# Kernel tuning notes

Hardware: AMD Instinct MI355X
Metric: run time of the kernel (lower is better)

The kernel has to match this reference:

```python
import jax, jax.numpy as jnp
import numpy as np
import math

EPS = 0.0001

def _filterbank(delta, center, image_size, glimpse_size):
    # delta, center: (B,) in [-1,1]. Returns (B, glimpse_size, image_size),
    # matching torch _get_filterbanks output fx.transpose(1,2).
    centers = (image_size - 1.0) * (center + 1.0) / 2.0            # (B,)
    deltas = (float(image_size) / glimpse_size) * (1.0 - jnp.abs(delta))
    gammas = jnp.exp(1.0 - 2.0 * jnp.abs(delta))                   # (B,)
    gp = jnp.arange(glimpse_size, dtype=jnp.float32) - (glimpse_size - 1.0) / 2.0
    mu = centers[:, None] + deltas[:, None] * gp[None, :]          # (B, g)
    ip = jnp.arange(image_size, dtype=jnp.float32)                 # (I,)
    fx = (ip[None, None, :] - mu[:, :, None]) / gammas[:, None, None]  # (B, g, I)
    fx = 1.0 / (math.pi * gammas[:, None, None] * (1.0 + fx * fx))
    fx = fx / (jnp.sum(fx, axis=2, keepdims=True) + EPS)
    return fx


def setup_inputs() -> dict:
    key = jax.random.key(0)
    ks = jax.random.split(key, 7)
    B, C, H, W = 64, 3, 256, 256
    gh, gw, co = 16, 16, 512
    in_dim = gh * gw * C
    s_ih = 1.0 / np.sqrt(co)
    return {
        "image_pairs": jax.random.normal(ks[0], (B, 2, C, H, W), dtype=jnp.float32),
        "W_ih": jax.random.normal(ks[1], (4 * co, in_dim), dtype=jnp.float32) * s_ih,
        "W_hh": jax.random.normal(ks[2], (4 * co, co), dtype=jnp.float32) * s_ih,
        "b_ih": jax.random.normal(ks[3], (4 * co,), dtype=jnp.float32) * s_ih,
        "b_hh": jax.random.normal(ks[4], (4 * co,), dtype=jnp.float32) * s_ih,
        "Wg": jax.random.normal(ks[5], (3, co), dtype=jnp.float32) * 0.05,
        "bg": jax.random.normal(ks[6], (3,), dtype=jnp.float32) * 0.05,
        "num_glimpses": 8,
    }


def reference(image_pairs, W_ih, W_hh, b_ih, b_hh, Wg, bg, num_glimpses):
    B, _, C, H, W = image_pairs.shape
    co = W_hh.shape[1]
    gh = gw = 16

    def step(carry, turn):
        h, c = carry
        img = image_pairs[:, turn % 2]                 # (B, C, H, W)
        gp = jnp.tanh(h @ Wg.T + bg)                   # (B, 3)
        Fh = _filterbank(gp[:, 2], gp[:, 0], H, gh)    # (B, gh, H)
        Fw = _filterbank(gp[:, 2], gp[:, 1], W, gw)    # (B, gw, W)
        # glimpse = Fh @ img @ Fw^T per channel -> (B, C, gh, gw)
        g = jnp.einsum('bgh,bchw->bcgw', Fh, img)
        g = jnp.einsum('bcgw,bkw->bcgk', g, Fw)
        x = g.reshape(B, -1)                           # (B, C*gh*gw)
        gates = x @ W_ih.T + b_ih + h @ W_hh.T + b_hh  # (B, 4*co)
        i, f, gg, o = jnp.split(gates, 4, axis=1)
        c_new = jax.nn.sigmoid(f) * c + jax.nn.sigmoid(i) * jnp.tanh(gg)
        h_new = jax.nn.sigmoid(o) * jnp.tanh(c_new)
        return (h_new, c_new), h_new

    h0 = jnp.zeros((B, co), dtype=jnp.float32)
    c0 = jnp.zeros((B, co), dtype=jnp.float32)
    (hT, _), _ = jax.lax.scan(step, (h0, c0), jnp.arange(2 * num_glimpses))
    return hT
```

## Files before the change

kernel.cpp:

```cpp
#include <hip/hip_runtime.h>
#include <math.h>

#define NB 64
#define CO 512
#define NGATES 2048
#define INDIM 768
#define KTOT 1280
#define IMG 256
#define GS 16
#define EPSF 1e-4f
#define NCHUNK 8
#define CHUNK 160

#define FMA4(A,S,V) {(A).x+=(S)*(V).x;(A).y+=(S)*(V).y;(A).z+=(S)*(V).z;(A).w+=(S)*(V).w;}

__device__ __forceinline__ float sigmoidf_(float x){ return 1.0f/(1.0f+expf(-x)); }

__device__ __forceinline__ float waveReduceSum(float v){
  #pragma unroll
  for (int off=32; off>0; off>>=1) v += __shfl_down(v, off, 64);
  return v;
}

__global__ __launch_bounds__(256) void transpose_k(const float* __restrict__ in,
                                                   float* __restrict__ out,
                                                   int rows, int cols){
  __shared__ float tile[32][33];
  int bx = blockIdx.x*32, by = blockIdx.y*32;
  int tx = threadIdx.x, ty = threadIdx.y;
  #pragma unroll
  for (int i=ty;i<32;i+=8)
    tile[i][tx] = in[(size_t)(by+i)*cols + bx+tx];
  __syncthreads();
  #pragma unroll
  for (int i=ty;i<32;i+=8)
    out[(size_t)(bx+i)*rows + by+tx] = tile[tx][i];
}

__global__ __launch_bounds__(512) void extlstm4_k(
    const float* __restrict__ imgs, int t,
    const float* __restrict__ partT,
    const float* __restrict__ b_ih, const float* __restrict__ b_hh,
    const float* __restrict__ Wg,   const float* __restrict__ bg,
    float* __restrict__ cbuf, float* __restrict__ xhT)
{
  __shared__ float hs[CO];
  __shared__ float gp[3];
  __shared__ float wred[8][4];
  __shared__ float prt[2][GS][4];
  __shared__ float rowinv[2][GS];
  __shared__ float fhT[256][20];
  __shared__ float fws[GS][260];
  __shared__ float g1[4][GS][260];
  __shared__ float g2[256][2];

  const int bc = blockIdx.x;
  const int b = bc/3, c = bc%3;
  const int t0 = threadIdx.x;
  const int q = t0>>6, lane = t0&63;

  if (t == 0){
    if (t0 < 256){ hs[t0]=0.f; hs[t0+256]=0.f; }
    if (c == 0) xhT[(size_t)(INDIM+t0)*NB + b] = 0.f;
  } else {
    const int u = t0;
    float gi=0.f,gf=0.f,gc=0.f,go=0.f;
    #pragma unroll
    for (int s2=0;s2<NCHUNK;s2++){
      const float* p = partT + ((size_t)s2*NB + b)*NGATES;
      gi += p[u]; gf += p[512+u]; gc += p[1024+u]; go += p[1536+u];
    }
    gi += b_ih[u]      + b_hh[u];
    gf += b_ih[512+u]  + b_hh[512+u];
    gc += b_ih[1024+u] + b_hh[1024+u];
    go += b_ih[1536+u] + b_hh[1536+u];
    float cold = (t==1) ? 0.f : cbuf[(size_t)((t-1)&1)*NB*CO + (size_t)b*CO + u];
    float cnew = sigmoidf_(gf)*cold + sigmoidf_(gi)*tanhf(gc);
    float hnew = sigmoidf_(go)*tanhf(cnew);
    hs[u] = hnew;
    if (c == 0){
      cbuf[(size_t)(t&1)*NB*CO + (size_t)b*CO + u] = cnew;
      xhT[(size_t)(INDIM+u)*NB + b] = hnew;
    }
  }
  __syncthreads();

  {
    float hval = hs[t0];
    float p0 = Wg[0*CO+t0]*hval;
    float p1 = Wg[1*CO+t0]*hval;
    float p2 = Wg[2*CO+t0]*hval;
    p0 = waveReduceSum(p0); p1 = waveReduceSum(p1); p2 = waveReduceSum(p2);
    if (lane==0){ wred[q][0]=p0; wred[q][1]=p1; wred[q][2]=p2; }
    __syncthreads();
    if (t0 < 3){
      float s = 0.f;
      #pragma unroll
      for (int w8=0; w8<8; w8++) s += wred[w8][t0];
      gp[t0] = tanhf(s + bg[t0]);
    }
    __syncthreads();
  }

  {
    float delta = gp[2];
    float dabs  = fabsf(delta);
    float deltas = ((float)IMG/(float)GS) * (1.0f - dabs);
    float gamma  = expf(1.0f - 2.0f*dabs);
    float inv_g  = 1.0f/gamma;
    float pref   = 1.0f/(3.14159265358979f*gamma);
    const int fb = t0 >> 8;
    const int p  = t0 & 255;
    const int wid = q & 3;
    float fi = (float)p;
    float fx[GS];
    float centers = 255.0f*0.5f*(gp[fb]+1.0f);
    #pragma unroll
    for (int g=0; g<GS; g++){
      float mu = centers + deltas*((float)g - 7.5f);
      float d  = (fi - mu)*inv_g;
      fx[g] = pref/(1.0f + d*d);
    }
    #pragma unroll
    for (int g=0; g<GS; g++){
      float sv = waveReduceSum(fx[g]);
      if (lane==0) prt[fb][g][wid]=sv;
    }
    __syncthreads();
    if (t0 < 32){
      int f2 = t0 >> 4, g = t0 & 15;
      rowinv[f2][g] = 1.0f/((((prt[f2][g][0]+prt[f2][g][1])+prt[f2][g][2])+prt[f2][g][3]) + EPSF);
    }
    __syncthreads();
    if (fb==0){
      #pragma unroll
      for (int g=0; g<GS; g++) fhT[p][g] = fx[g]*rowinv[0][g];
    } else {
      #pragma unroll
      for (int g=0; g<GS; g++) fws[g][p] = fx[g]*rowinv[1][g];
    }
    __syncthreads();
  }

  {
    const float4* img4 = (const float4*)(imgs
        + (((size_t)b*2 + (t&1))*3 + c)*((size_t)IMG*IMG));
    float4 acc[GS];
    #pragma unroll
    for (int g=0; g<GS; g++){ acc[g].x=0.f; acc[g].y=0.f; acc[g].z=0.f; acc[g].w=0.f; }
    const int row0 = q*32;
    #pragma unroll 8
    for (int i=0; i<32; i++){
      const int row = row0 + i;
      float4 v = img4[(size_t)row*64 + lane];
      const float4* fq = (const float4*)&fhT[row][0];
      float4 f0=fq[0], f1=fq[1], f2=fq[2], f3=fq[3];
      FMA4(acc[0], f0.x, v); FMA4(acc[1], f0.y, v); FMA4(acc[2], f0.z, v); FMA4(acc[3], f0.w, v);
      FMA4(acc[4], f1.x, v); FMA4(acc[5], f1.y, v); FMA4(acc[6], f1.z, v); FMA4(acc[7], f1.w, v);
      FMA4(acc[8], f2.x, v); FMA4(acc[9], f2.y, v); FMA4(acc[10],f2.z, v); FMA4(acc[11],f2.w, v);
      FMA4(acc[12],f3.x, v); FMA4(acc[13],f3.y, v); FMA4(acc[14],f3.z, v); FMA4(acc[15],f3.w, v);
    }
    if (q < 4){
      #pragma unroll
      for (int g=0; g<GS; g++) *(float4*)&g1[q][g][lane*4] = acc[g];
    }
    __syncthreads();
    if (q >= 4){
      #pragma unroll
      for (int g=0; g<GS; g++){
        float4 o = *(float4*)&g1[q-4][g][lane*4];
        o.x+=acc[g].x; o.y+=acc[g].y; o.z+=acc[g].z; o.w+=acc[g].w;
        *(float4*)&g1[q-4][g][lane*4] = o;
      }
    }
    __syncthreads();
    {
      #pragma unroll
      for (int gi2=0; gi2<2; gi2++){
        int g = q*2 + gi2;
        float4 s0 = *(float4*)&g1[0][g][lane*4];
        float4 s1 = *(float4*)&g1[1][g][lane*4];
        float4 s2 = *(float4*)&g1[2][g][lane*4];
        float4 s3 = *(float4*)&g1[3][g][lane*4];
        s0.x = ((s0.x+s1.x)+s2.x)+s3.x;
        s0.y = ((s0.y+s1.y)+s2.y)+s3.y;
        s0.z = ((s0.z+s1.z)+s2.z)+s3.z;
        s0.w = ((s0.w+s1.w)+s2.w)+s3.w;
        *(float4*)&g1[0][g][lane*4] = s0;
      }
    }
    __syncthreads();
  }

  {
    int h2 = q >> 2;
    int o  = (q & 3)*64 + lane;
    int gg = o >> 4, kk = o & 15;
    const float4* grow = (const float4*)&g1[0][gg][h2*128];
    const float4* frow = (const float4*)&fws[kk][h2*128];
    float s = 0.f;
    #pragma unroll 8
    for (int j=0; j<32; j++){
      float4 gv = grow[j], fv = frow[j];
      s += gv.x*fv.x; s += gv.y*fv.y; s += gv.z*fv.z; s += gv.w*fv.w;
    }
    g2[o][h2] = s;
    __syncthreads();
    if (t0 < 256)
      xhT[(size_t)(c*256 + t0)*NB + b] = g2[t0][0] + g2[t0][1];
  }
}

__global__ __launch_bounds__(256) void gates8_k(
    const float* __restrict__ Wcat,
    const float* __restrict__ xhT,
    float* __restrict__ partT)
{
  __shared__ float Wlds[CHUNK][32];
  __shared__ float xhl[CHUNK][NB];
  const int s  = blockIdx.x & (NCHUNK-1);
  const int rt = blockIdx.x >> 3;
  const int r0 = rt*32;
  const int c0 = s*CHUNK;
  const int t  = threadIdx.x;

  {
    const float* wsrc = Wcat + (size_t)c0*NGATES + r0;
    const int f4 = t & 7, kk = t >> 3;
    #pragma unroll
    for (int p=0; p<5; p++){
      const int k = kk + p*32;
      *(float4*)&Wlds[k][f4*4] =
          *(const float4*)(wsrc + (size_t)k*NGATES + f4*4);
    }
    const float4* xsrc = (const float4*)(xhT + (size_t)c0*NB);
    float4* xdst = (float4*)&xhl[0][0];
    #pragma unroll
    for (int p=0; p<10; p++)
      xdst[t + p*256] = xsrc[t + p*256];
  }
  __syncthreads();

  const int r4 = t & 7, bp = t >> 3;
  float a00=0.f,a01=0.f,a10=0.f,a11=0.f,a20=0.f,a21=0.f,a30=0.f,a31=0.f;
  #pragma unroll 8
  for (int k=0; k<CHUNK; k++){
    float4 w = *(const float4*)&Wlds[k][r4*4];
    float2 x = *(const float2*)&xhl[k][bp*2];
    a00+=w.x*x.x; a01+=w.x*x.y;
    a10+=w.y*x.x; a11+=w.y*x.y;
    a20+=w.z*x.x; a21+=w.z*x.y;
    a30+=w.w*x.x; a31+=w.w*x.y;
  }
  __syncthreads();

  float* tile = &xhl[0][0];
  const int rl = r4*4, bb = bp*2;
  tile[(rl+0)*65 + bb] = a00; tile[(rl+0)*65 + bb+1] = a01;
  tile[(rl+1)*65 + bb] = a10; tile[(rl+1)*65 + bb+1] = a11;
  tile[(rl+2)*65 + bb] = a20; tile[(rl+2)*65 + bb+1] = a21;
  tile[(rl+3)*65 + bb] = a30; tile[(rl+3)*65 + bb+1] = a31;
  __syncthreads();
  const int b = t >> 2, qq = t & 3;
  float* dst = partT + ((size_t)s*NB + b)*NGATES + r0 + qq*8;
  float4 v0, v1;
  v0.x=tile[(qq*8+0)*65+b]; v0.y=tile[(qq*8+1)*65+b];
  v0.z=tile[(qq*8+2)*65+b]; v0.w=tile[(qq*8+3)*65+b];
  v1.x=tile[(qq*8+4)*65+b]; v1.y=tile[(qq*8+5)*65+b];
  v1.z=tile[(qq*8+6)*65+b]; v1.w=tile[(qq*8+7)*65+b];
  *(float4*)dst = v0;
  *(float4*)(dst+4) = v1;
}

__global__ __launch_bounds__(512) void final_k(
    const float* __restrict__ partT,
    const float* __restrict__ b_ih, const float* __restrict__ b_hh,
    const float* __restrict__ cbuf, float* __restrict__ out)
{
  int b = blockIdx.x, u = threadIdx.x;
  float gi=0.f, gf=0.f, gc=0.f, go=0.f;
  #pragma unroll
  for (int s2=0; s2<NCHUNK; s2++){
    const float* p = partT + ((size_t)s2*NB + b)*NGATES;
    gi += p[u]; gf += p[512+u]; gc += p[1024+u]; go += p[1536+u];
  }
  gi += b_ih[u]      + b_hh[u];
  gf += b_ih[512+u]  + b_hh[512+u];
  gc += b_ih[1024+u] + b_hh[1024+u];
  go += b_ih[1536+u] + b_hh[1536+u];
  float cold = cbuf[(size_t)1*NB*CO + (size_t)b*CO + u];
  float cnew = sigmoidf_(gf)*cold + sigmoidf_(gi)*tanhf(gc);
  float hnew = sigmoidf_(go)*tanhf(cnew);
  out[(size_t)b*CO + u] = hnew;
}

extern "C" void kernel_launch(void* const* d_in, const int* in_sizes, int n_in,
                              void* d_out, int out_size, void* d_ws, size_t ws_size,
                              hipStream_t stream){
  const float* imgs = (const float*)d_in[0];
  const float* W_ih = (const float*)d_in[1];
  const float* W_hh = (const float*)d_in[2];
  const float* b_ih = (const float*)d_in[3];
  const float* b_hh = (const float*)d_in[4];
  const float* Wg   = (const float*)d_in[5];
  const float* bg   = (const float*)d_in[6];

  float* ws = (float*)d_ws;
  size_t off = 0;
  float* Wcat  = ws + off; off += (size_t)KTOT*NGATES;
  float* xhT   = ws + off; off += (size_t)KTOT*NB;
  float* partT = ws + off; off += (size_t)NCHUNK*NB*NGATES;
  float* cbuf  = ws + off; off += (size_t)2*NB*CO;
  float* outp  = (float*)d_out;

  transpose_k<<<dim3(INDIM/32, NGATES/32), dim3(32,8), 0, stream>>>(W_ih, Wcat, NGATES, INDIM);
  transpose_k<<<dim3(CO/32,    NGATES/32), dim3(32,8), 0, stream>>>(W_hh, Wcat + (size_t)INDIM*NGATES, NGATES, CO);

  for (int t=0; t<16; t++){
    extlstm4_k<<<NB*3, 512, 0, stream>>>(imgs, t, partT, b_ih, b_hh, Wg, bg, cbuf, xhT);
    gates8_k  <<<512,  256, 0, stream>>>(Wcat, xhT, partT);
  }
  final_k<<<NB, 512, 0, stream>>>(partT, b_ih, b_hh, cbuf, outp);
}
```

Measured before the change: 522.6 us.

## Split LSTM cell update into separate kernel and prefetch image rows in glimpse kernel

Moves the LSTM gate reduction and cell update out of the glimpse kernel into its own small kernel, so the three per-channel blocks no longer each recompute it, and passes h through a global buffer. The glimpse kernel gets a launch-bounds occupancy hint and fully unrolls its row loop with a 16-deep register prefetch buffer for image loads. The final kernel is folded into the new reduction kernel. The cost is an extra kernel launch per step and higher register pressure from the prefetch buffer.

```diff
diff --git a/kernel.cpp b/kernel.cpp
--- a/kernel.cpp
+++ b/kernel.cpp
@@ -37,14 +37,49 @@
     out[(size_t)(bx+i)*rows + by+tx] = tile[tx][i];
 }
 
-__global__ __launch_bounds__(512) void extlstm4_k(
-    const float* __restrict__ imgs, int t,
+__global__ __launch_bounds__(128) void lstmred_k(
+    int t,
     const float* __restrict__ partT,
     const float* __restrict__ b_ih, const float* __restrict__ b_hh,
-    const float* __restrict__ Wg,   const float* __restrict__ bg,
-    float* __restrict__ cbuf, float* __restrict__ xhT)
+    float* __restrict__ cbuf,
+    float* __restrict__ hbuf,
+    float* __restrict__ xhT,
+    float* __restrict__ out)
 {
-  __shared__ float hs[CO];
+  const int b = blockIdx.x >> 2;
+  const int u = (blockIdx.x & 3)*128 + threadIdx.x;
+  if (t == 0){
+    hbuf[(size_t)b*CO + u] = 0.f;
+    xhT[(size_t)(INDIM+u)*NB + b] = 0.f;
+    return;
+  }
+  float gi=0.f,gf=0.f,gc=0.f,go=0.f;
+  #pragma unroll
+  for (int s2=0;s2<NCHUNK;s2++){
+    const float* p = partT + ((size_t)s2*NB + b)*NGATES;
+    gi += p[u]; gf += p[512+u]; gc += p[1024+u]; go += p[1536+u];
+  }
+  gi += b_ih[u]      + b_hh[u];
+  gf += b_ih[512+u]  + b_hh[512+u];
+  gc += b_ih[1024+u] + b_hh[1024+u];
+  go += b_ih[1536+u] + b_hh[1536+u];
+  float cold = (t==1) ? 0.f : cbuf[(size_t)((t-1)&1)*NB*CO + (size_t)b*CO + u];
+  float cnew = sigmoidf_(gf)*cold + sigmoidf_(gi)*tanhf(gc);
+  float hnew = sigmoidf_(go)*tanhf(cnew);
+  cbuf[(size_t)(t&1)*NB*CO + (size_t)b*CO + u] = cnew;
+  hbuf[(size_t)b*CO + u] = hnew;
+  if (t < 16) xhT[(size_t)(INDIM+u)*NB + b] = hnew;
+  else        out[(size_t)b*CO + u] = hnew;
+}
+
+__global__ __launch_bounds__(512, 2) void extlstm7_k(
+    const float* __restrict__ imgs,
+    int t,
+    const float* __restrict__ hbuf,
+    const float* __restrict__ Wg,
+    const float* __restrict__ bg,
+    float* __restrict__ xhT)
+{
   __shared__ float gp[3];
   __shared__ float wred[8][4];
   __shared__ float prt[2][GS][4];
@@ -59,34 +94,8 @@
   const int t0 = threadIdx.x;
   const int q = t0>>6, lane = t0&63;
 
-  if (t == 0){
-    if (t0 < 256){ hs[t0]=0.f; hs[t0+256]=0.f; }
-    if (c == 0) xhT[(size_t)(INDIM+t0)*NB + b] = 0.f;
-  } else {
-    const int u = t0;
-    float gi=0.f,gf=0.f,gc=0.f,go=0.f;
-    #pragma unroll
-    for (int s2=0;s2<NCHUNK;s2++){
-      const float* p = partT + ((size_t)s2*NB + b)*NGATES;
-      gi += p[u]; gf += p[512+u]; gc += p[1024+u]; go += p[1536+u];
-    }
-    gi += b_ih[u]      + b_hh[u];
-    gf += b_ih[512+u]  + b_hh[512+u];
-    gc += b_ih[1024+u] + b_hh[1024+u];
-    go += b_ih[1536+u] + b_hh[1536+u];
-    float cold = (t==1) ? 0.f : cbuf[(size_t)((t-1)&1)*NB*CO + (size_t)b*CO + u];
-    float cnew = sigmoidf_(gf)*cold + sigmoidf_(gi)*tanhf(gc);
-    float hnew = sigmoidf_(go)*tanhf(cnew);
-    hs[u] = hnew;
-    if (c == 0){
-      cbuf[(size_t)(t&1)*NB*CO + (size_t)b*CO + u] = cnew;
-      xhT[(size_t)(INDIM+u)*NB + b] = hnew;
-    }
-  }
-  __syncthreads();
-
-  {
-    float hval = hs[t0];
+  {
+    float hval = hbuf[(size_t)b*CO + t0];
     float p0 = Wg[0*CO+t0]*hval;
     float p1 = Wg[1*CO+t0]*hval;
     float p2 = Wg[2*CO+t0]*hval;
@@ -149,11 +158,15 @@
     #pragma unroll
     for (int g=0; g<GS; g++){ acc[g].x=0.f; acc[g].y=0.f; acc[g].z=0.f; acc[g].w=0.f; }
     const int row0 = q*32;
-    #pragma unroll 8
+    const float4* ip = img4 + (size_t)row0*64 + lane;
+    float4 vb[16];
+    #pragma unroll
+    for (int p0=0; p0<16; p0++) vb[p0] = ip[(size_t)p0*64];
+    #pragma unroll
     for (int i=0; i<32; i++){
-      const int row = row0 + i;
-      float4 v = img4[(size_t)row*64 + lane];
-      const float4* fq = (const float4*)&fhT[row][0];
+      float4 v = vb[i & 15];
+      if (i + 16 < 32) vb[i & 15] = ip[(size_t)(i+16)*64];
+      const float4* fq = (const float4*)&fhT[row0 + i][0];
       float4 f0=fq[0], f1=fq[1], f2=fq[2], f3=fq[3];
       FMA4(acc[0], f0.x, v); FMA4(acc[1], f0.y, v); FMA4(acc[2], f0.z, v); FMA4(acc[3], f0.w, v);
       FMA4(acc[4], f1.x, v); FMA4(acc[5], f1.y, v); FMA4(acc[6], f1.z, v); FMA4(acc[7], f1.w, v);
@@ -272,28 +285,6 @@
   *(float4*)(dst+4) = v1;
 }
 
-__global__ __launch_bounds__(512) void final_k(
-    const float* __restrict__ partT,
-    const float* __restrict__ b_ih, const float* __restrict__ b_hh,
-    const float* __restrict__ cbuf, float* __restrict__ out)
-{
-  int b = blockIdx.x, u = threadIdx.x;
-  float gi=0.f, gf=0.f, gc=0.f, go=0.f;
-  #pragma unroll
-  for (int s2=0; s2<NCHUNK; s2++){
-    const float* p = partT + ((size_t)s2*NB + b)*NGATES;
-    gi += p[u]; gf += p[512+u]; gc += p[1024+u]; go += p[1536+u];
-  }
-  gi += b_ih[u]      + b_hh[u];
-  gf += b_ih[512+u]  + b_hh[512+u];
-  gc += b_ih[1024+u] + b_hh[1024+u];
-  go += b_ih[1536+u] + b_hh[1536+u];
-  float cold = cbuf[(size_t)1*NB*CO + (size_t)b*CO + u];
-  float cnew = sigmoidf_(gf)*cold + sigmoidf_(gi)*tanhf(gc);
-  float hnew = sigmoidf_(go)*tanhf(cnew);
-  out[(size_t)b*CO + u] = hnew;
-}
-
 extern "C" void kernel_launch(void* const* d_in, const int* in_sizes, int n_in,
                               void* d_out, int out_size, void* d_ws, size_t ws_size,
                               hipStream_t stream){
@@ -311,14 +302,16 @@
   float* xhT   = ws + off; off += (size_t)KTOT*NB;
   float* partT = ws + off; off += (size_t)NCHUNK*NB*NGATES;
   float* cbuf  = ws + off; off += (size_t)2*NB*CO;
+  float* hbuf  = ws + off; off += (size_t)NB*CO;
   float* outp  = (float*)d_out;
 
   transpose_k<<<dim3(INDIM/32, NGATES/32), dim3(32,8), 0, stream>>>(W_ih, Wcat, NGATES, INDIM);
   transpose_k<<<dim3(CO/32,    NGATES/32), dim3(32,8), 0, stream>>>(W_hh, Wcat + (size_t)INDIM*NGATES, NGATES, CO);
 
   for (int t=0; t<16; t++){
-    extlstm4_k<<<NB*3, 512, 0, stream>>>(imgs, t, partT, b_ih, b_hh, Wg, bg, cbuf, xhT);
+    lstmred_k <<<NB*4, 128, 0, stream>>>(t, partT, b_ih, b_hh, cbuf, hbuf, xhT, outp);
+    extlstm7_k<<<NB*3, 512, 0, stream>>>(imgs, t, hbuf, Wg, bg, xhT);
     gates8_k  <<<512,  256, 0, stream>>>(Wcat, xhT, partT);
   }
-  final_k<<<NB, 512, 0, stream>>>(partT, b_ih, b_hh, cbuf, outp);
-}
+  lstmred_k<<<NB*4, 128, 0, stream>>>(16, partT, b_ih, b_hh, cbuf, hbuf, xhT, outp);
+}
```

Result: slower. 547.7 us (+4.8%).
